# Performance work log

Hardware: AMD Instinct MI355X
Metric: run time of the kernel (lower is better)

## Reference

```python
import jax, jax.numpy as jnp
import numpy as np

N, F, D, E, L, T = 20000, 512, 256, 200000, 3, 2  # nodes, raw feat, hidden, edges/etype, layers, etypes


def _layernorm(x, g, b, eps=1e-5):
    mu = jnp.mean(x, axis=-1, keepdims=True)
    var = jnp.mean(jnp.square(x - mu), axis=-1, keepdims=True)
    return (x - mu) * jax.lax.rsqrt(var + eps) * g + b


def setup_inputs() -> dict:
    key = jax.random.key(0)
    ks = jax.random.split(key, 12)
    s = 0.02
    return {
        "x": jax.random.normal(ks[0], (N, F), dtype=jnp.float32),
        "src": jax.random.randint(ks[1], (T, E), 0, N, dtype=jnp.int32),
        "dst": jax.random.randint(ks[2], (T, E), 0, N, dtype=jnp.int32),
        # HeteroLinear (single ntype)
        "Wlin": jax.random.normal(ks[3], (D, F), dtype=jnp.float32) * s,
        "blin": jnp.zeros((D,), dtype=jnp.float32),
        # stacked per-layer, per-etype SAGEConv('pool') params
        "Wpool": jax.random.normal(ks[4], (L, T, D, D), dtype=jnp.float32) * s,
        "bpool": jnp.zeros((L, T, D), dtype=jnp.float32),
        "Wself": jax.random.normal(ks[5], (L, T, D, D), dtype=jnp.float32) * s,
        "Wneigh": jax.random.normal(ks[6], (L, T, D, D), dtype=jnp.float32) * s,
        "bconv": jnp.zeros((L, T, D), dtype=jnp.float32),
        "gamma": jnp.ones((L, T, D), dtype=jnp.float32),
        "beta": jnp.zeros((L, T, D), dtype=jnp.float32),
    }


def reference(x, src, dst, Wlin, blin, Wpool, bpool, Wself, Wneigh, bconv, gamma, beta):
    n = x.shape[0]
    # HeteroLinear: raw features -> embed
    h = x @ Wlin.T + blin
    for l in range(L):
        out = None
        for t in range(T):  # per edge-type SAGEConv, aggregator='pool'
            hp = jax.nn.relu(h @ Wpool[l, t].T + bpool[l, t])        # fc_pool + relu on src nodes
            m = hp[src[t]]                                            # gather [E, D]
            neigh = jax.ops.segment_max(m, dst[t], num_segments=n)    # max-pool reduce
            neigh = jnp.where(jnp.isneginf(neigh), 0.0, neigh)        # zero-in-degree -> 0 (DGL)
            rst = h @ Wself[l, t].T + neigh @ Wneigh[l, t].T + bconv[l, t]
            if l < L - 1:
                rst = jax.nn.relu(rst)                                # activation before norm
            rst = _layernorm(rst, gamma[l, t], beta[l, t])
            out = rst if out is None else out + rst                   # HeteroGraphConv 'sum'
        h = out
    return h
```

## Files before the change

### kernel.cpp

```cpp
#include <hip/hip_runtime.h>

#define N_NODES 20000
#define F_IN    512
#define D_H     256
#define E_EDGES 200000
#define L_LAYERS 3
#define T_ETYPES 2

typedef __attribute__((ext_vector_type(8))) short bf16x8;
typedef __attribute__((ext_vector_type(4))) float f32x4;

__device__ __forceinline__ unsigned short f2b(float f) {
    unsigned int u = __float_as_uint(f);
    u = (u + 0x7FFFu + ((u >> 16) & 1u)) >> 16;
    return (unsigned short)u;
}
__device__ __forceinline__ unsigned int pack2(float a, float b) {
    return (unsigned int)f2b(a) | ((unsigned int)f2b(b) << 16);
}

__device__ __forceinline__ void gload16(const unsigned short* g, unsigned short* l)
{
    __builtin_amdgcn_global_load_lds(
        (const __attribute__((address_space(1))) void*)g,
        (__attribute__((address_space(3))) void*)l, 16, 0, 0);
}

__device__ __forceinline__ void shufg8(const float* __restrict__ s,
                                       unsigned short* __restrict__ d,
                                       int NO, int K, int o8)
{
    const int matsz8 = (NO * K) >> 3;
    const int mat = o8 / matsz8;
    const int rem = o8 - mat * matsz8;
    const int dst = rem << 3;
    const int slab = dst >> 12;
    const int w = dst & 4095;
    const int spr = K >> 5;
    const int slab_n = slab / spr, slab_k = slab - slab_n * spr;
    const int nl = (((w >> 9) & 7) << 4) + ((w >> 3) & 15);
    const int kk = ((w >> 7) & 3) << 3;
    const size_t soff = (size_t)mat * NO * K + (size_t)(slab_n * 128 + nl) * K
                      + slab_k * 32 + kk;
    const float4 a = *(const float4*)(s + soff);
    const float4 b = *(const float4*)(s + soff + 4);
    uint4 u;
    u.x = pack2(a.x, a.y); u.y = pack2(a.z, a.w);
    u.z = pack2(b.x, b.y); u.w = pack2(b.z, b.w);
    *(uint4*)(d + (size_t)mat * NO * K + dst) = u;
}

__global__ __launch_bounds__(256) void prep_kernel(
    const float* __restrict__ x,  unsigned short* __restrict__ xb, int nx8,
    const float* __restrict__ s0, unsigned short* __restrict__ d0, int NO0, int K0, int n08,
    const float* __restrict__ s1, unsigned short* __restrict__ d1, int NO1, int K1, int n18,
    const float* __restrict__ s2, unsigned short* __restrict__ d2, int NO2, int K2, int n28,
    const float* __restrict__ s3, unsigned short* __restrict__ d3, int NO3, int K3, int n38)
{
    int i = blockIdx.x * 256 + threadIdx.x;
    if (i < nx8) {
        const float4 a = ((const float4*)x)[i * 2];
        const float4 b = ((const float4*)x)[i * 2 + 1];
        uint4 u;
        u.x = pack2(a.x, a.y); u.y = pack2(a.z, a.w);
        u.z = pack2(b.x, b.y); u.w = pack2(b.z, b.w);
        ((uint4*)xb)[i] = u;
        return;
    }
    i -= nx8;
    if (i < n08) { shufg8(s0, d0, NO0, K0, i); return; }
    if ((i -= n08) < n18) { shufg8(s1, d1, NO1, K1, i); return; }
    if ((i -= n18) < n28) { shufg8(s2, d2, NO2, K2, i); return; }
    if ((i -= n28) < n38) { shufg8(s3, d3, NO3, K3, i); return; }
}

template <int NSTEPS, int CS>
__global__ __launch_bounds__(512) void gemm_lds(
    const unsigned short* __restrict__ A,
    const unsigned short* __restrict__ Wf,
    const float* __restrict__ bias, unsigned short* __restrict__ Cout,
    int M, int ldc, int relu)
{
    __shared__ __align__(16) unsigned short As[3][4096];
    __shared__ __align__(16) unsigned short Bs[3][4096];
    const int K = NSTEPS * 32;
    const int tid = threadIdx.x, lane = tid & 63;
    const int w = tid >> 6, wm = w >> 2, wn = w & 3;
    const int id = blockIdx.x;
    const int g = id / (8 * CS), rem = id - g * (8 * CS);
    const int cs = rem >> 3, bmi = (g << 3) | (rem & 7);
    const int MB = (M + 127) >> 7;
    if (bmi >= MB) return;
    const int bm = bmi * 128;
    const unsigned short* slab0 = Wf + (((size_t)cs * NSTEPS) << 12);

    const int rg = min(bm + ((tid >> 6) << 4) + (tid & 15), M - 1);
    const size_t aoff = (size_t)rg * K + ((tid >> 4) & 3) * 8;
    const unsigned short* bsrc = slab0 + (size_t)tid * 8;

    const int cbase = cs * 128 + wn * 32 + (lane & 15);
    float bj[2];
#pragma unroll
    for (int j = 0; j < 2; ++j) bj[j] = bias[cbase + j * 16];
    asm volatile("" ::: "memory");

    f32x4 acc[4][2] = {};

#define GL_STAGE(S, BUF) do { \
    gload16(A + aoff + (S) * 32, &As[BUF][(size_t)tid * 8]); \
    gload16(bsrc + (((size_t)(S)) << 12), &Bs[BUF][(size_t)tid * 8]); \
} while (0)

    GL_STAGE(0, 0);
    GL_STAGE(1, 1);
#pragma unroll
    for (int s = 0; s < NSTEPS; ++s) {
        if (s + 1 < NSTEPS) asm volatile("s_waitcnt vmcnt(2)" ::: "memory");
        else                asm volatile("s_waitcnt vmcnt(0)" ::: "memory");
        __builtin_amdgcn_s_barrier();
        asm volatile("" ::: "memory");
        if (s + 2 < NSTEPS) GL_STAGE(s + 2, (s + 2) % 3);
        const int buf = s % 3;
        bf16x8 a[4], b[2];
#pragma unroll
        for (int mi = 0; mi < 4; ++mi)
            a[mi] = *(const bf16x8*)((const char*)As[buf] + ((wm * 4 + mi) << 10) + lane * 16);
#pragma unroll
        for (int j = 0; j < 2; ++j)
            b[j] = *(const bf16x8*)((const char*)Bs[buf] + ((wn * 2 + j) << 10) + lane * 16);
#pragma unroll
        for (int mi = 0; mi < 4; ++mi)
#pragma unroll
            for (int j = 0; j < 2; ++j)
                acc[mi][j] = __builtin_amdgcn_mfma_f32_16x16x32_bf16(a[mi], b[j], acc[mi][j], 0, 0, 0);
    }
#undef GL_STAGE

    const int rb = bm + wm * 64 + ((lane >> 4) << 2);
#pragma unroll
    for (int j = 0; j < 2; ++j) {
#pragma unroll
        for (int mi = 0; mi < 4; ++mi)
#pragma unroll
            for (int r = 0; r < 4; ++r) {
                const int row = rb + mi * 16 + r;
                if (row < M) {
                    float v = acc[mi][j][r] + bj[j];
                    if (relu) v = fmaxf(v, 0.f);
                    Cout[(size_t)row * ldc + cbase + j * 16] = f2b(v);
                }
            }
    }
}

template <int RELU>
__global__ __launch_bounds__(512) void tail_gemm(
    const unsigned short* __restrict__ h,
    const unsigned short* __restrict__ neigh,
    const unsigned short* __restrict__ Ws,
    const unsigned short* __restrict__ Wn,
    const float* __restrict__ bias,
    float* __restrict__ R)
{
    __shared__ __align__(16) unsigned short As[3][4096];
    __shared__ __align__(16) unsigned short Bs[3][4096];
    const int tid = threadIdx.x, lane = tid & 63;
    const int w = tid >> 6, wm = w >> 2, wn = w & 3;
    const int id = blockIdx.x;
    const int g = id >> 5, rem = id & 31;
    const int cs = rem >> 3, bmi = (g << 3) | (rem & 7);
    const int MB = (N_NODES + 127) >> 7;
    if (bmi >= MB) return;
    const int bm = bmi * 128;
    const int e  = cs >> 1;
    const unsigned short* Bself  = Ws + (size_t)e * 65536 + (cs & 1) * 32768;
    const unsigned short* Bneigh = Wn + (size_t)e * 65536 + (cs & 1) * 32768;

    const int rg = min(bm + ((tid >> 6) << 4) + (tid & 15), N_NODES - 1);
    const size_t aoffH = (size_t)rg * 256 + ((tid >> 4) & 3) * 8;
    const size_t aoffN = (size_t)rg * 512 + e * 256 + ((tid >> 4) & 3) * 8;

    const int cbase = cs * 128 + wn * 32 + (lane & 15);
    float bj[2];
#pragma unroll
    for (int j = 0; j < 2; ++j) bj[j] = bias[cbase + j * 16];
    asm volatile("" ::: "memory");

    f32x4 acc[4][2] = {};

#define TG_STAGE(S, BUF) do { \
    const unsigned short* as_ = ((S) < 8) ? (h + aoffH + (S) * 32) \
                                          : (neigh + aoffN + ((S) - 8) * 32); \
    gload16(as_, &As[BUF][(size_t)tid * 8]); \
    const unsigned short* bs_ = (((S) < 8) ? (Bself + (S) * 4096) \
                                           : (Bneigh + ((S) - 8) * 4096)) \
                                + (size_t)tid * 8; \
    gload16(bs_, &Bs[BUF][(size_t)tid * 8]); \
} while (0)

    TG_STAGE(0, 0);
    TG_STAGE(1, 1);
#pragma unroll
    for (int s = 0; s < 16; ++s) {
        if (s + 1 < 16) asm volatile("s_waitcnt vmcnt(2)" ::: "memory");
        else            asm volatile("s_waitcnt vmcnt(0)" ::: "memory");
        __builtin_amdgcn_s_barrier();
        asm volatile("" ::: "memory");
        if (s + 2 < 16) TG_STAGE(s + 2, (s + 2) % 3);
        const int buf = s % 3;
        bf16x8 a[4], b[2];
#pragma unroll
        for (int mi = 0; mi < 4; ++mi)
            a[mi] = *(const bf16x8*)((const char*)As[buf] + ((wm * 4 + mi) << 10) + lane * 16);
#pragma unroll
        for (int j = 0; j < 2; ++j)
            b[j] = *(const bf16x8*)((const char*)Bs[buf] + ((wn * 2 + j) << 10) + lane * 16);
#pragma unroll
        for (int mi = 0; mi < 4; ++mi)
#pragma unroll
            for (int j = 0; j < 2; ++j)
                acc[mi][j] = __builtin_amdgcn_mfma_f32_16x16x32_bf16(a[mi], b[j], acc[mi][j], 0, 0, 0);
    }
#undef TG_STAGE

    const int rb = bm + wm * 64 + ((lane >> 4) << 2);
#pragma unroll
    for (int j = 0; j < 2; ++j) {
#pragma unroll
        for (int mi = 0; mi < 4; ++mi)
#pragma unroll
            for (int r = 0; r < 4; ++r) {
                const int row = rb + mi * 16 + r;
                if (row < N_NODES) {
                    float v = acc[mi][j][r] + bj[j];
                    if (RELU) v = fmaxf(v, 0.f);
                    R[(size_t)row * 512 + cbase + j * 16] = v;
                }
            }
    }
}

template <int LAST>
__global__ __launch_bounds__(256) void ln_sum_kernel(
    const float* __restrict__ R,
    const float* __restrict__ gamma,
    const float* __restrict__ beta,
    void* __restrict__ outp)
{
    const int row  = blockIdx.x * 4 + (threadIdx.x >> 6);
    const int lane = threadIdx.x & 63;
    const float4 v0 = ((const float4*)R)[(size_t)row * 128 + lane];
    const float4 v1 = ((const float4*)R)[(size_t)row * 128 + 64 + lane];
    float s0 = v0.x + v0.y + v0.z + v0.w;
    float q0 = v0.x * v0.x + v0.y * v0.y + v0.z * v0.z + v0.w * v0.w;
    float s1 = v1.x + v1.y + v1.z + v1.w;
    float q1 = v1.x * v1.x + v1.y * v1.y + v1.z * v1.z + v1.w * v1.w;
#pragma unroll
    for (int o = 1; o < 64; o <<= 1) {
        s0 += __shfl_xor(s0, o); q0 += __shfl_xor(q0, o);
        s1 += __shfl_xor(s1, o); q1 += __shfl_xor(q1, o);
    }
    const float m0 = s0 * (1.f / 256.f), m1 = s1 * (1.f / 256.f);
    const float i0 = rsqrtf(q0 * (1.f / 256.f) - m0 * m0 + 1e-5f);
    const float i1 = rsqrtf(q1 * (1.f / 256.f) - m1 * m1 + 1e-5f);
    const float4 g0 = ((const float4*)gamma)[lane];
    const float4 b0 = ((const float4*)beta)[lane];
    const float4 g1 = ((const float4*)(gamma + 256))[lane];
    const float4 b1 = ((const float4*)(beta + 256))[lane];
    const float o0 = (v0.x - m0) * i0 * g0.x + b0.x + (v1.x - m1) * i1 * g1.x + b1.x;
    const float o1 = (v0.y - m0) * i0 * g0.y + b0.y + (v1.y - m1) * i1 * g1.y + b1.y;
    const float o2 = (v0.z - m0) * i0 * g0.z + b0.z + (v1.z - m1) * i1 * g1.z + b1.z;
    const float o3 = (v0.w - m0) * i0 * g0.w + b0.w + (v1.w - m1) * i1 * g1.w + b1.w;
    if (LAST) {
        ((float4*)outp)[(size_t)row * 64 + lane] = make_float4(o0, o1, o2, o3);
    } else {
        ushort4 u;
        u.x = f2b(o0); u.y = f2b(o1); u.z = f2b(o2); u.w = f2b(o3);
        ((ushort4*)outp)[(size_t)row * 64 + lane] = u;
    }
}

__global__ __launch_bounds__(256) void count_deg_kernel(
    const int* __restrict__ dst, int* __restrict__ cnt, int E2)
{
    int e = blockIdx.x * 256 + threadIdx.x;
    if (e < E2) {
        const int base = (e >= E_EDGES) ? N_NODES : 0;
        atomicAdd(&cnt[base + dst[e]], 1);
    }
}

__global__ __launch_bounds__(256) void scanA_kernel(
    const int* __restrict__ cnt, int* __restrict__ incl, int* __restrict__ bsum, int n)
{
    __shared__ int tmp[256];
    const int tid = threadIdx.x;
    const int i = blockIdx.x * 256 + tid;
    const int v = (i < n) ? cnt[i] : 0;
    tmp[tid] = v;
    __syncthreads();
#pragma unroll
    for (int o = 1; o < 256; o <<= 1) {
        const int t = (tid >= o) ? tmp[tid - o] : 0;
        __syncthreads();
        tmp[tid] += t;
        __syncthreads();
    }
    if (i < n) incl[i] = tmp[tid];
    if (tid == 255) bsum[blockIdx.x] = tmp[255];
}

__global__ __launch_bounds__(256) void scanB_kernel(int* __restrict__ bsum, int nb)
{
    __shared__ int tmp[256];
    const int tid = threadIdx.x;
    const int v = (tid < nb) ? bsum[tid] : 0;
    tmp[tid] = v;
    __syncthreads();
#pragma unroll
    for (int o = 1; o < 256; o <<= 1) {
        const int t = (tid >= o) ? tmp[tid - o] : 0;
        __syncthreads();
        tmp[tid] += t;
        __syncthreads();
    }
    if (tid < nb) bsum[tid] = tmp[tid] - v;
}

__global__ __launch_bounds__(256) void scanC_kernel(
    const int* __restrict__ cnt, const int* __restrict__ incl,
    const int* __restrict__ bsum, int* __restrict__ off, int* __restrict__ cursor, int n)
{
    const int i = blockIdx.x * 256 + threadIdx.x;
    if (i < n) {
        const int e = incl[i] + bsum[blockIdx.x];
        off[i + 1] = e;
        cursor[i] = e - cnt[i];
    }
    if (i == 0) off[0] = 0;
}

__global__ __launch_bounds__(256) void fill_csr_kernel(
    const int* __restrict__ src, const int* __restrict__ dst,
    int* __restrict__ cursor, int* __restrict__ esrc, int E2)
{
    int e = blockIdx.x * 256 + threadIdx.x;
    if (e < E2) {
        const int base = (e >= E_EDGES) ? N_NODES : 0;
        const int pos = atomicAdd(&cursor[base + dst[e]], 1);
        esrc[pos] = src[e];
    }
}

__device__ __forceinline__ ushort4 umax4(ushort4 a, ushort4 b)
{
    a.x = a.x > b.x ? a.x : b.x;
    a.y = a.y > b.y ? a.y : b.y;
    a.z = a.z > b.z ? a.z : b.z;
    a.w = a.w > b.w ? a.w : b.w;
    return a;
}

__global__ __launch_bounds__(256) void seg_max_kernel(
    const unsigned short* __restrict__ hp, const int* __restrict__ off,
    const int* __restrict__ esrc, unsigned short* __restrict__ neigh)
{
    const int g = blockIdx.x * 4 + (threadIdx.x >> 6);
    if (g >= 2 * N_NODES) return;
    const int t = (g >= N_NODES) ? 1 : 0;
    const int node = g - t * N_NODES;
    const int lane = threadIdx.x & 63;
    const int co = t * D_H + lane * 4;
    const int e0 = off[g], e1 = off[g + 1];
    ushort4 acc = make_ushort4(0, 0, 0, 0);
    int e = e0;
    for (; e + 4 <= e1; e += 4) {
        const int s0 = esrc[e + 0], s1 = esrc[e + 1];
        const int s2 = esrc[e + 2], s3 = esrc[e + 3];
        const ushort4 v0 = *(const ushort4*)(hp + (size_t)s0 * 512 + co);
        const ushort4 v1 = *(const ushort4*)(hp + (size_t)s1 * 512 + co);
        const ushort4 v2 = *(const ushort4*)(hp + (size_t)s2 * 512 + co);
        const ushort4 v3 = *(const ushort4*)(hp + (size_t)s3 * 512 + co);
        acc = umax4(umax4(umax4(acc, v0), umax4(v1, v2)), v3);
    }
    for (; e < e1; ++e)
        acc = umax4(acc, *(const ushort4*)(hp + (size_t)esrc[e] * 512 + co));
    *(ushort4*)(neigh + (size_t)node * 512 + co) = acc;
}

extern "C" void kernel_launch(void* const* d_in, const int* in_sizes, int n_in,
                              void* d_out, int out_size, void* d_ws, size_t ws_size,
                              hipStream_t stream)
{
    const float* x      = (const float*)d_in[0];
    const int*   src    = (const int*)d_in[1];
    const int*   dst    = (const int*)d_in[2];
    const float* Wlin   = (const float*)d_in[3];
    const float* blin   = (const float*)d_in[4];
    const float* Wpool  = (const float*)d_in[5];
    const float* bpool  = (const float*)d_in[6];
    const float* Wself  = (const float*)d_in[7];
    const float* Wneigh = (const float*)d_in[8];
    const float* bconv  = (const float*)d_in[9];
    const float* gamma  = (const float*)d_in[10];
    const float* beta   = (const float*)d_in[11];

    const size_t NB = (size_t)N_NODES * D_H;
    char* p = (char*)d_ws;
    unsigned short* hp_b    = (unsigned short*)p; p += NB * 2 * T_ETYPES;
    unsigned short* neigh_b = (unsigned short*)p; p += NB * 2 * T_ETYPES;
    unsigned short* h_a     = (unsigned short*)p; p += NB * 2;
    unsigned short* h_b     = (unsigned short*)p; p += NB * 2;
    unsigned short* xb      = (unsigned short*)p; p += (size_t)N_NODES * F_IN * 2;
    float*          Rbuf    = (float*)p;          p += (size_t)N_NODES * 512 * 4;
    unsigned short* wlin_f  = (unsigned short*)p; p += (size_t)D_H * F_IN * 2;
    const size_t WSZ = (size_t)L_LAYERS * T_ETYPES * D_H * D_H;
    unsigned short* wpool_f = (unsigned short*)p; p += WSZ * 2;
    unsigned short* wself_f = (unsigned short*)p; p += WSZ * 2;
    unsigned short* wneigh_f= (unsigned short*)p; p += WSZ * 2;
    int* ip = (int*)p;
    const int NT = T_ETYPES * N_NODES;
    int* cnt    = ip; ip += NT;
    int* incl   = ip; ip += NT;
    int* off    = ip; ip += NT + 1;
    int* cursor = ip; ip += NT;
    int* esrc   = ip; ip += T_ETYPES * E_EDGES;
    int* bsum   = ip; ip += 256;

    const dim3 blk(256);
    const dim3 blk512(512);
    const int E2 = T_ETYPES * E_EDGES;
    const dim3 e2grid((E2 + 255) / 256);
    const int nScanBlk = (NT + 255) / 256;

    {
        const int nx8  = N_NODES * F_IN / 8;
        const int nl8  = D_H * F_IN / 8;
        const int nw8  = (int)(WSZ / 8);
        const int tot  = nx8 + nl8 + 3 * nw8;
        prep_kernel<<<dim3((tot + 255) / 256), blk, 0, stream>>>(
            x, xb, nx8,
            Wlin, wlin_f, D_H, F_IN, nl8,
            Wpool, wpool_f, T_ETYPES * D_H, D_H, nw8,
            Wself, wself_f, D_H, D_H, nw8,
            Wneigh, wneigh_f, D_H, D_H, nw8);
    }

    hipMemsetAsync(cnt, 0, (size_t)NT * sizeof(int), stream);
    count_deg_kernel<<<e2grid, blk, 0, stream>>>(dst, cnt, E2);
    scanA_kernel<<<dim3(nScanBlk), blk, 0, stream>>>(cnt, incl, bsum, NT);
    scanB_kernel<<<dim3(1), blk, 0, stream>>>(bsum, nScanBlk);
    scanC_kernel<<<dim3(nScanBlk), blk, 0, stream>>>(cnt, incl, bsum, off, cursor, NT);
    fill_csr_kernel<<<e2grid, blk, 0, stream>>>(src, dst, cursor, esrc, E2);

    const int MGRP = ((N_NODES + 127) / 128 + 7) / 8;

    gemm_lds<16, 2><<<dim3(MGRP * 16), blk512, 0, stream>>>(
        xb, wlin_f, blin, h_a, N_NODES, D_H, 0);

    unsigned short* h = h_a;
    unsigned short* hn = h_b;
    const dim3 sgrid((2 * N_NODES + 3) / 4);
    const dim3 lngrid(N_NODES / 4);
    for (int l = 0; l < L_LAYERS; ++l) {
        gemm_lds<8, 4><<<dim3(MGRP * 32), blk512, 0, stream>>>(
            h, wpool_f + (size_t)l * T_ETYPES * D_H * D_H,
            bpool + (size_t)l * T_ETYPES * D_H, hp_b, N_NODES, T_ETYPES * D_H, 1);
        seg_max_kernel<<<sgrid, blk, 0, stream>>>(hp_b, off, esrc, neigh_b);
        const size_t wlo = (size_t)l * T_ETYPES * D_H * D_H;
        const size_t blo = (size_t)l * T_ETYPES * D_H;
        if (l < L_LAYERS - 1) {
            tail_gemm<1><<<dim3(MGRP * 32), blk512, 0, stream>>>(
                h, neigh_b, wself_f + wlo, wneigh_f + wlo, bconv + blo, Rbuf);
            ln_sum_kernel<0><<<lngrid, blk, 0, stream>>>(
                Rbuf, gamma + blo, beta + blo, hn);
        } else {
            tail_gemm<0><<<dim3(MGRP * 32), blk512, 0, stream>>>(
                h, neigh_b, wself_f + wlo, wneigh_f + wlo, bconv + blo, Rbuf);
            ln_sum_kernel<1><<<lngrid, blk, 0, stream>>>(
                Rbuf, gamma + blo, beta + blo, d_out);
        }
        unsigned short* tmp = h; h = hn; hn = tmp;
    }
}
```

Before: 390.6 us.

## Store GEMM A-operands in pre-swizzled slab layout and merge scan kernels

Activations (x, h, neigh) are now written in the same 128x32 slab-tiled layout the MFMA GEMMs load into LDS. Each global_load_lds then reads one contiguous 4 KB block instead of strided row segments, and producer kernels (prep, layernorm, seg_max, first GEMM) write through a slab address function. Buffers are padded to a multiple of 128 rows. Separately, the three-kernel prefix scan is replaced by a single-block serial-chunk scan, which cuts launches but serializes about 157 chunks on one workgroup.

```diff
diff --git a/kernel.cpp b/kernel.cpp
--- a/kernel.cpp
+++ b/kernel.cpp
@@ -6,6 +6,8 @@
 #define E_EDGES 200000
 #define L_LAYERS 3
 #define T_ETYPES 2
+#define NBANDS  157
+#define M_PAD   (NBANDS * 128)
 
 typedef __attribute__((ext_vector_type(8))) short bf16x8;
 typedef __attribute__((ext_vector_type(4))) float f32x4;
@@ -26,9 +28,16 @@
         (__attribute__((address_space(3))) void*)l, 16, 0, 0);
 }
 
+__device__ __forceinline__ size_t slab_addr(int row, int col, int kslabs)
+{
+    return ((size_t)(row >> 7) * kslabs + (col >> 5)) * 4096
+         + (((row >> 4) & 7) << 9) + (((col >> 3) & 3) << 7)
+         + ((row & 15) << 3) + (col & 7);
+}
+
 __device__ __forceinline__ void shufg8(const float* __restrict__ s,
                                        unsigned short* __restrict__ d,
-                                       int NO, int K, int o8)
+                                       int NO, int Mreal, int K, int o8)
 {
     const int matsz8 = (NO * K) >> 3;
     const int mat = o8 / matsz8;
@@ -38,10 +47,10 @@
     const int w = dst & 4095;
     const int spr = K >> 5;
     const int slab_n = slab / spr, slab_k = slab - slab_n * spr;
-    const int nl = (((w >> 9) & 7) << 4) + ((w >> 3) & 15);
+    int row = slab_n * 128 + (((w >> 9) & 7) << 4) + ((w >> 3) & 15);
+    if (row >= Mreal) row = Mreal - 1;
     const int kk = ((w >> 7) & 3) << 3;
-    const size_t soff = (size_t)mat * NO * K + (size_t)(slab_n * 128 + nl) * K
-                      + slab_k * 32 + kk;
+    const size_t soff = (size_t)mat * Mreal * K + (size_t)row * K + slab_k * 32 + kk;
     const float4 a = *(const float4*)(s + soff);
     const float4 b = *(const float4*)(s + soff + 4);
     uint4 u;
@@ -58,23 +67,15 @@
     const float* __restrict__ s3, unsigned short* __restrict__ d3, int NO3, int K3, int n38)
 {
     int i = blockIdx.x * 256 + threadIdx.x;
-    if (i < nx8) {
-        const float4 a = ((const float4*)x)[i * 2];
-        const float4 b = ((const float4*)x)[i * 2 + 1];
-        uint4 u;
-        u.x = pack2(a.x, a.y); u.y = pack2(a.z, a.w);
-        u.z = pack2(b.x, b.y); u.w = pack2(b.z, b.w);
-        ((uint4*)xb)[i] = u;
-        return;
-    }
+    if (i < nx8) { shufg8(x, xb, M_PAD, N_NODES, F_IN, i); return; }
     i -= nx8;
-    if (i < n08) { shufg8(s0, d0, NO0, K0, i); return; }
-    if ((i -= n08) < n18) { shufg8(s1, d1, NO1, K1, i); return; }
-    if ((i -= n18) < n28) { shufg8(s2, d2, NO2, K2, i); return; }
-    if ((i -= n28) < n38) { shufg8(s3, d3, NO3, K3, i); return; }
-}
-
-template <int NSTEPS, int CS>
+    if (i < n08) { shufg8(s0, d0, NO0, NO0, K0, i); return; }
+    if ((i -= n08) < n18) { shufg8(s1, d1, NO1, NO1, K1, i); return; }
+    if ((i -= n18) < n28) { shufg8(s2, d2, NO2, NO2, K2, i); return; }
+    if ((i -= n28) < n38) { shufg8(s3, d3, NO3, NO3, K3, i); return; }
+}
+
+template <int NSTEPS, int CS, int SLABOUT>
 __global__ __launch_bounds__(512) void gemm_lds(
     const unsigned short* __restrict__ A,
     const unsigned short* __restrict__ Wf,
@@ -83,7 +84,6 @@
 {
     __shared__ __align__(16) unsigned short As[3][4096];
     __shared__ __align__(16) unsigned short Bs[3][4096];
-    const int K = NSTEPS * 32;
     const int tid = threadIdx.x, lane = tid & 63;
     const int w = tid >> 6, wm = w >> 2, wn = w & 3;
     const int id = blockIdx.x;
@@ -93,9 +93,7 @@
     if (bmi >= MB) return;
     const int bm = bmi * 128;
     const unsigned short* slab0 = Wf + (((size_t)cs * NSTEPS) << 12);
-
-    const int rg = min(bm + ((tid >> 6) << 4) + (tid & 15), M - 1);
-    const size_t aoff = (size_t)rg * K + ((tid >> 4) & 3) * 8;
+    const unsigned short* abase = A + (((size_t)bmi * NSTEPS) << 12) + (size_t)tid * 8;
     const unsigned short* bsrc = slab0 + (size_t)tid * 8;
 
     const int cbase = cs * 128 + wn * 32 + (lane & 15);
@@ -107,7 +105,7 @@
     f32x4 acc[4][2] = {};
 
 #define GL_STAGE(S, BUF) do { \
-    gload16(A + aoff + (S) * 32, &As[BUF][(size_t)tid * 8]); \
+    gload16(abase + (((size_t)(S)) << 12), &As[BUF][(size_t)tid * 8]); \
     gload16(bsrc + (((size_t)(S)) << 12), &Bs[BUF][(size_t)tid * 8]); \
 } while (0)
 
@@ -147,7 +145,10 @@
                 if (row < M) {
                     float v = acc[mi][j][r] + bj[j];
                     if (relu) v = fmaxf(v, 0.f);
-                    Cout[(size_t)row * ldc + cbase + j * 16] = f2b(v);
+                    if (SLABOUT)
+                        Cout[slab_addr(row, cbase + j * 16, 8)] = f2b(v);
+                    else
+                        Cout[(size_t)row * ldc + cbase + j * 16] = f2b(v);
                 }
             }
     }
@@ -169,16 +170,13 @@
     const int id = blockIdx.x;
     const int g = id >> 5, rem = id & 31;
     const int cs = rem >> 3, bmi = (g << 3) | (rem & 7);
-    const int MB = (N_NODES + 127) >> 7;
-    if (bmi >= MB) return;
+    if (bmi >= NBANDS) return;
     const int bm = bmi * 128;
     const int e  = cs >> 1;
     const unsigned short* Bself  = Ws + (size_t)e * 65536 + (cs & 1) * 32768;
     const unsigned short* Bneigh = Wn + (size_t)e * 65536 + (cs & 1) * 32768;
-
-    const int rg = min(bm + ((tid >> 6) << 4) + (tid & 15), N_NODES - 1);
-    const size_t aoffH = (size_t)rg * 256 + ((tid >> 4) & 3) * 8;
-    const size_t aoffN = (size_t)rg * 512 + e * 256 + ((tid >> 4) & 3) * 8;
+    const unsigned short* ah = h + (((size_t)bmi * 8) << 12) + (size_t)tid * 8;
+    const unsigned short* an = neigh + (((size_t)bmi * 16 + e * 8) << 12) + (size_t)tid * 8;
 
     const int cbase = cs * 128 + wn * 32 + (lane & 15);
     float bj[2];
@@ -189,11 +187,11 @@
     f32x4 acc[4][2] = {};
 
 #define TG_STAGE(S, BUF) do { \
-    const unsigned short* as_ = ((S) < 8) ? (h + aoffH + (S) * 32) \
-                                          : (neigh + aoffN + ((S) - 8) * 32); \
+    const unsigned short* as_ = ((S) < 8) ? (ah + (((size_t)(S)) << 12)) \
+                                          : (an + (((size_t)((S) - 8)) << 12)); \
     gload16(as_, &As[BUF][(size_t)tid * 8]); \
-    const unsigned short* bs_ = (((S) < 8) ? (Bself + (S) * 4096) \
-                                           : (Bneigh + ((S) - 8) * 4096)) \
+    const unsigned short* bs_ = (((S) < 8) ? (Bself + ((S) << 12)) \
+                                           : (Bneigh + (((S) - 8) << 12))) \
                                 + (size_t)tid * 8; \
     gload16(bs_, &Bs[BUF][(size_t)tid * 8]); \
 } while (0)
@@ -276,7 +274,7 @@
     } else {
         ushort4 u;
         u.x = f2b(o0); u.y = f2b(o1); u.z = f2b(o2); u.w = f2b(o3);
-        ((ushort4*)outp)[(size_t)row * 64 + lane] = u;
+        *(ushort4*)((unsigned short*)outp + slab_addr(row, lane * 4, 8)) = u;
     }
 }
 
@@ -290,54 +288,32 @@
     }
 }
 
-__global__ __launch_bounds__(256) void scanA_kernel(
-    const int* __restrict__ cnt, int* __restrict__ incl, int* __restrict__ bsum, int n)
+__global__ __launch_bounds__(256) void scan_kernel(
+    const int* __restrict__ cnt, int* __restrict__ off, int* __restrict__ cursor, int n)
 {
     __shared__ int tmp[256];
+    __shared__ int carry_s;
     const int tid = threadIdx.x;
-    const int i = blockIdx.x * 256 + tid;
-    const int v = (i < n) ? cnt[i] : 0;
-    tmp[tid] = v;
+    if (tid == 0) { carry_s = 0; off[0] = 0; }
     __syncthreads();
-#pragma unroll
-    for (int o = 1; o < 256; o <<= 1) {
-        const int t = (tid >= o) ? tmp[tid - o] : 0;
+    for (int base = 0; base < n; base += 256) {
+        const int i = base + tid;
+        const int v = (i < n) ? cnt[i] : 0;
+        tmp[tid] = v;
         __syncthreads();
-        tmp[tid] += t;
+#pragma unroll
+        for (int o = 1; o < 256; o <<= 1) {
+            const int t = (tid >= o) ? tmp[tid - o] : 0;
+            __syncthreads();
+            tmp[tid] += t;
+            __syncthreads();
+        }
+        const int incl = tmp[tid] + carry_s;
+        if (i < n) { off[i + 1] = incl; cursor[i] = incl - v; }
         __syncthreads();
-    }
-    if (i < n) incl[i] = tmp[tid];
-    if (tid == 255) bsum[blockIdx.x] = tmp[255];
-}
-
-__global__ __launch_bounds__(256) void scanB_kernel(int* __restrict__ bsum, int nb)
-{
-    __shared__ int tmp[256];
-    const int tid = threadIdx.x;
-    const int v = (tid < nb) ? bsum[tid] : 0;
-    tmp[tid] = v;
-    __syncthreads();
-#pragma unroll
-    for (int o = 1; o < 256; o <<= 1) {
-        const int t = (tid >= o) ? tmp[tid - o] : 0;
+        if (tid == 255) carry_s += tmp[255];
         __syncthreads();
-        tmp[tid] += t;
-        __syncthreads();
-    }
-    if (tid < nb) bsum[tid] = tmp[tid] - v;
-}
-
-__global__ __launch_bounds__(256) void scanC_kernel(
-    const int* __restrict__ cnt, const int* __restrict__ incl,
-    const int* __restrict__ bsum, int* __restrict__ off, int* __restrict__ cursor, int n)
-{
-    const int i = blockIdx.x * 256 + threadIdx.x;
-    if (i < n) {
-        const int e = incl[i] + bsum[blockIdx.x];
-        off[i + 1] = e;
-        cursor[i] = e - cnt[i];
-    }
-    if (i == 0) off[0] = 0;
+    }
 }
 
 __global__ __launch_bounds__(256) void fill_csr_kernel(
@@ -385,7 +361,7 @@
     }
     for (; e < e1; ++e)
         acc = umax4(acc, *(const ushort4*)(hp + (size_t)esrc[e] * 512 + co));
-    *(ushort4*)(neigh + (size_t)node * 512 + co) = acc;
+    *(ushort4*)(neigh + slab_addr(node, co, 16)) = acc;
 }
 
 extern "C" void kernel_launch(void* const* d_in, const int* in_sizes, int n_in,
@@ -405,13 +381,12 @@
     const float* gamma  = (const float*)d_in[10];
     const float* beta   = (const float*)d_in[11];
 
-    const size_t NB = (size_t)N_NODES * D_H;
     char* p = (char*)d_ws;
-    unsigned short* hp_b    = (unsigned short*)p; p += NB * 2 * T_ETYPES;
-    unsigned short* neigh_b = (unsigned short*)p; p += NB * 2 * T_ETYPES;
-    unsigned short* h_a     = (unsigned short*)p; p += NB * 2;
-    unsigned short* h_b     = (unsigned short*)p; p += NB * 2;
-    unsigned short* xb      = (unsigned short*)p; p += (size_t)N_NODES * F_IN * 2;
+    unsigned short* hp_b    = (unsigned short*)p; p += (size_t)N_NODES * 512 * 2;
+    unsigned short* neigh_b = (unsigned short*)p; p += (size_t)M_PAD * 512 * 2;
+    unsigned short* h_a     = (unsigned short*)p; p += (size_t)M_PAD * 256 * 2;
+    unsigned short* h_b     = (unsigned short*)p; p += (size_t)M_PAD * 256 * 2;
+    unsigned short* xb      = (unsigned short*)p; p += (size_t)M_PAD * F_IN * 2;
     float*          Rbuf    = (float*)p;          p += (size_t)N_NODES * 512 * 4;
     unsigned short* wlin_f  = (unsigned short*)p; p += (size_t)D_H * F_IN * 2;
     const size_t WSZ = (size_t)L_LAYERS * T_ETYPES * D_H * D_H;
@@ -421,20 +396,17 @@
     int* ip = (int*)p;
     const int NT = T_ETYPES * N_NODES;
     int* cnt    = ip; ip += NT;
-    int* incl   = ip; ip += NT;
     int* off    = ip; ip += NT + 1;
     int* cursor = ip; ip += NT;
     int* esrc   = ip; ip += T_ETYPES * E_EDGES;
-    int* bsum   = ip; ip += 256;
 
     const dim3 blk(256);
     const dim3 blk512(512);
     const int E2 = T_ETYPES * E_EDGES;
     const dim3 e2grid((E2 + 255) / 256);
-    const int nScanBlk = (NT + 255) / 256;
 
     {
-        const int nx8  = N_NODES * F_IN / 8;
+        const int nx8  = M_PAD * F_IN / 8;
         const int nl8  = D_H * F_IN / 8;
         const int nw8  = (int)(WSZ / 8);
         const int tot  = nx8 + nl8 + 3 * nw8;
@@ -448,14 +420,12 @@
 
     hipMemsetAsync(cnt, 0, (size_t)NT * sizeof(int), stream);
     count_deg_kernel<<<e2grid, blk, 0, stream>>>(dst, cnt, E2);
-    scanA_kernel<<<dim3(nScanBlk), blk, 0, stream>>>(cnt, incl, bsum, NT);
-    scanB_kernel<<<dim3(1), blk, 0, stream>>>(bsum, nScanBlk);
-    scanC_kernel<<<dim3(nScanBlk), blk, 0, stream>>>(cnt, incl, bsum, off, cursor, NT);
+    scan_kernel<<<dim3(1), blk, 0, stream>>>(cnt, off, cursor, NT);
     fill_csr_kernel<<<e2grid, blk, 0, stream>>>(src, dst, cursor, esrc, E2);
 
-    const int MGRP = ((N_NODES + 127) / 128 + 7) / 8;
-
-    gemm_lds<16, 2><<<dim3(MGRP * 16), blk512, 0, stream>>>(
+    const int MGRP = (NBANDS + 7) / 8;
+
+    gemm_lds<16, 2, 1><<<dim3(MGRP * 16), blk512, 0, stream>>>(
         xb, wlin_f, blin, h_a, N_NODES, D_H, 0);
 
     unsigned short* h = h_a;
@@ -463,7 +433,7 @@
     const dim3 sgrid((2 * N_NODES + 3) / 4);
     const dim3 lngrid(N_NODES / 4);
     for (int l = 0; l < L_LAYERS; ++l) {
-        gemm_lds<8, 4><<<dim3(MGRP * 32), blk512, 0, stream>>>(
+        gemm_lds<8, 4, 0><<<dim3(MGRP * 32), blk512, 0, stream>>>(
             h, wpool_f + (size_t)l * T_ETYPES * D_H * D_H,
             bpool + (size_t)l * T_ETYPES * D_H, hp_b, N_NODES, T_ETYPES * D_H, 1);
         seg_max_kernel<<<sgrid, blk, 0, stream>>>(hp_b, off, esrc, neigh_b);
```

Result: slower. 549.1 us (+40.6%).
